# Kernel optimization log

Hardware: AMD Instinct MI355X
Metric: run time of the kernel (lower is better)

Reference implementation:

```python
import jax, jax.numpy as jnp
import numpy as np

N_CLASSES = 80
SEG_LEN = 512          # boxes per class (uniform segments)
H = 128                # hidden_size
DH = 2 * H             # decoder hidden (= concat of bidirectional encoder final hiddens)
EMB = 32               # decoder_input_dim
SOS, EOS = 2, 3


def _gru_cell(x, h, Wih, Whh, bih, bhh):
    # PyTorch GRU cell math. x:(in,), h:(hid,), Wih:(3*hid,in), Whh:(3*hid,hid)
    gi = Wih @ x + bih
    gh = Whh @ h + bhh
    i_r, i_z, i_n = jnp.split(gi, 3)
    h_r, h_z, h_n = jnp.split(gh, 3)
    r = jax.nn.sigmoid(i_r + h_r)
    z = jax.nn.sigmoid(i_z + h_z)
    n = jnp.tanh(i_n + r * h_n)
    return (1.0 - z) * n + z * h


def _gru_seq(xs, h0, Wih, Whh, bih, bhh):
    # xs: (T, in); returns final hidden (hid,) and all hiddens (T, hid)
    def step(h, x):
        h2 = _gru_cell(x, h, Wih, Whh, bih, bhh)
        return h2, h2
    hT, hs = jax.lax.scan(step, h0, xs)
    return hT, hs

# vmap over the 80 classes (per-class weights)
_run_gru = jax.vmap(_gru_seq, in_axes=(0, 0, 0, 0, 0, 0))


def setup_inputs() -> dict:
    key = jax.random.key(0)
    ks = jax.random.split(key, 32)
    N = N_CLASSES * SEG_LEN
    s = 0.05
    inp = {
        "feat": jax.random.normal(ks[0], (N, 1024), jnp.float32),
        "score": jax.random.uniform(ks[1], (N, 1), jnp.float32),
        "box": jax.random.uniform(ks[2], (N, 4), jnp.float32),
        "origin_score": jax.random.uniform(ks[3], (N, 91), jnp.float32),
        "labels": jax.random.randint(ks[4], (N,), 0, 2, jnp.int64),
        "weights": jax.random.uniform(ks[5], (N,), jnp.float32),
        "unique_class": jnp.ones((N_CLASSES,), jnp.int64),
        "unique_class_len": jnp.arange(N_CLASSES + 1, dtype=jnp.int64) * SEG_LEN,
        # shared linears
        "appear_W": jax.random.normal(ks[6], (H, 1024), jnp.float32) * s,
        "appear_b": jnp.zeros((H,), jnp.float32),
        "featlin_W": jax.random.normal(ks[7], (H, H + 96), jnp.float32) * s,
        "featlin_b": jnp.zeros((H,), jnp.float32),
        # per-class bidirectional encoder GRUs
        "enc_Wih_f": jax.random.normal(ks[8], (N_CLASSES, 3 * H, H), jnp.float32) * s,
        "enc_Whh_f": jax.random.normal(ks[9], (N_CLASSES, 3 * H, H), jnp.float32) * s,
        "enc_bih_f": jnp.zeros((N_CLASSES, 3 * H), jnp.float32),
        "enc_bhh_f": jnp.zeros((N_CLASSES, 3 * H), jnp.float32),
        "enc_Wih_b": jax.random.normal(ks[10], (N_CLASSES, 3 * H, H), jnp.float32) * s,
        "enc_Whh_b": jax.random.normal(ks[11], (N_CLASSES, 3 * H, H), jnp.float32) * s,
        "enc_bih_b": jnp.zeros((N_CLASSES, 3 * H), jnp.float32),
        "enc_bhh_b": jnp.zeros((N_CLASSES, 3 * H), jnp.float32),
        # decoder
        "dec_emb": jax.random.normal(ks[12], (4, EMB), jnp.float32) * s,
        "dec_Wih": jax.random.normal(ks[13], (N_CLASSES, 3 * DH, EMB), jnp.float32) * s,
        "dec_Whh": jax.random.normal(ks[14], (N_CLASSES, 3 * DH, DH), jnp.float32) * s,
        "dec_bih": jnp.zeros((N_CLASSES, 3 * DH), jnp.float32),
        "dec_bhh": jnp.zeros((N_CLASSES, 3 * DH), jnp.float32),
        "out_W": jax.random.normal(ks[15], (4, DH), jnp.float32) * s,
        "out_b": jnp.zeros((4,), jnp.float32),
    }
    return inp


def reference(feat, score, box, origin_score, labels, weights, unique_class,
              unique_class_len, appear_W, appear_b, featlin_W, featlin_b,
              enc_Wih_f, enc_Whh_f, enc_bih_f, enc_bhh_f,
              enc_Wih_b, enc_Whh_b, enc_bih_b, enc_bhh_b,
              dec_emb, dec_Wih, dec_Whh, dec_bih, dec_bhh, out_W, out_b):
    # --- shared feature encoding ---
    x = jax.nn.relu(feat @ appear_W.T + appear_b)                    # (N, H)
    allf = jnp.concatenate([x, score, box, origin_score], axis=1)    # (N, H+96)
    enc_feat = jax.nn.relu(allf @ featlin_W.T + featlin_b)           # (N, H)

    # --- per-class bidirectional encoder (uniform segments) ---
    seg = enc_feat.reshape(N_CLASSES, SEG_LEN, H)
    eos = jnp.ones((N_CLASSES, 1, H), enc_feat.dtype)                # encoder_EOS = ones
    enc_in = jnp.concatenate([seg, eos], axis=1)                     # (80, L+1, H)
    h0 = jnp.zeros((N_CLASSES, H), enc_feat.dtype)
    h_f, _ = _run_gru(enc_in, h0, enc_Wih_f, enc_Whh_f, enc_bih_f, enc_bhh_f)
    h_b, _ = _run_gru(enc_in[:, ::-1], h0, enc_Wih_b, enc_Whh_b, enc_bih_b, enc_bhh_b)
    dec_h0 = jnp.concatenate([h_f, h_b], axis=-1)                    # (80, 2H)

    # --- per-class decoder with teacher forcing (SOS then gold labels) ---
    emb = dec_emb[labels].reshape(N_CLASSES, SEG_LEN, EMB)
    sos = jnp.broadcast_to(dec_emb[SOS], (N_CLASSES, 1, EMB))
    dec_in = jnp.concatenate([sos, emb], axis=1)                     # (80, L+1, EMB)
    _, dec_hs = _run_gru(dec_in, dec_h0, dec_Wih, dec_Whh, dec_bih, dec_bhh)

    logits = dec_hs.reshape(-1, DH) @ out_W.T + out_b                # (80*(L+1), 4)
    output = jax.nn.log_softmax(logits, axis=-1)
    return output, labels, weights
```

## Files before the change

### kernel.cpp

```cpp
#include <hip/hip_runtime.h>


typedef __fp16 h2v __attribute__((ext_vector_type(2)));

#define HAVE_FDOT2 1

__device__ __forceinline__ h2v pk2(float a, float b) {
  return __builtin_amdgcn_cvt_pkrtz(a, b);
}
__device__ __forceinline__ unsigned h2u(h2v h) { return __builtin_bit_cast(unsigned, h); }
__device__ __forceinline__ h2v u2h(unsigned u) { return __builtin_bit_cast(h2v, u); }
__device__ __forceinline__ float fdot2f(h2v a, h2v b, float c) {
#if HAVE_FDOT2 && __has_builtin(__builtin_amdgcn_fdot2)
  return __builtin_amdgcn_fdot2(a, b, c, false);
#else
  return c + (float)a.x * (float)b.x + (float)a.y * (float)b.y;
#endif
}
__device__ __forceinline__ float sigf(float x) { return 1.f / (1.f + __expf(-x)); }
__device__ __forceinline__ float tanhfast(float x) { return 2.f / (1.f + __expf(-2.f * x)) - 1.f; }

__global__ void k_fill_misc(const float* __restrict__ score, const float* __restrict__ box,
                            const float* __restrict__ orig, float* __restrict__ allf) {
  int i = blockIdx.x * blockDim.x + threadIdx.x;
  if (i >= 40960 * 96) return;
  int row = i / 96, k = i - row * 96;
  float v;
  if (k == 0) v = score[row];
  else if (k < 5) v = box[row * 4 + (k - 1)];
  else v = orig[(size_t)row * 91 + (k - 5)];
  allf[(size_t)row * 224 + 128 + k] = v;
}

__global__ __launch_bounds__(256) void k_gemm_appear(
    const float* __restrict__ A, const float* __restrict__ W,
    const float* __restrict__ bias, float* __restrict__ allf) {
  __shared__ float As[32][68];
  __shared__ float Ws[32][132];
  const int tid = threadIdx.x;
  const int tx = tid & 15, ty = tid >> 4;
  const int r0 = blockIdx.x * 64;
  const int lr = tid >> 3;
  const int lk = (tid & 7) * 4;
  float acc[4][8];
#pragma unroll
  for (int i = 0; i < 4; ++i)
#pragma unroll
    for (int j = 0; j < 8; ++j) acc[i][j] = 0.f;

  for (int k0 = 0; k0 < 1024; k0 += 32) {
#pragma unroll
    for (int i = 0; i < 2; ++i) {
      int rr = lr + i * 32;
      float4 v = *(const float4*)(A + (size_t)(r0 + rr) * 1024 + k0 + lk);
      As[lk + 0][rr] = v.x; As[lk + 1][rr] = v.y; As[lk + 2][rr] = v.z; As[lk + 3][rr] = v.w;
    }
#pragma unroll
    for (int i = 0; i < 4; ++i) {
      int wr = lr + i * 32;
      float4 v = *(const float4*)(W + (size_t)wr * 1024 + k0 + lk);
      Ws[lk + 0][wr] = v.x; Ws[lk + 1][wr] = v.y; Ws[lk + 2][wr] = v.z; Ws[lk + 3][wr] = v.w;
    }
    __syncthreads();
#pragma unroll
    for (int kk = 0; kk < 32; ++kk) {
      float4 a = *(const float4*)&As[kk][ty * 4];
      float4 w0 = *(const float4*)&Ws[kk][tx * 8];
      float4 w1 = *(const float4*)&Ws[kk][tx * 8 + 4];
      float av[4] = {a.x, a.y, a.z, a.w};
      float wv[8] = {w0.x, w0.y, w0.z, w0.w, w1.x, w1.y, w1.z, w1.w};
#pragma unroll
      for (int i = 0; i < 4; ++i)
#pragma unroll
        for (int j = 0; j < 8; ++j) acc[i][j] = fmaf(av[i], wv[j], acc[i][j]);
    }
    __syncthreads();
  }
#pragma unroll
  for (int i = 0; i < 4; ++i) {
    int row = r0 + ty * 4 + i;
#pragma unroll
    for (int j = 0; j < 8; ++j) {
      int col = tx * 8 + j;
      float v = acc[i][j] + bias[col];
      allf[(size_t)row * 224 + col] = fmaxf(v, 0.f);
    }
  }
}

__global__ __launch_bounds__(256) void k_gemm_featlin(
    const float* __restrict__ A, const float* __restrict__ W,
    const float* __restrict__ bias, unsigned* __restrict__ encf2) {
  __shared__ float As[32][68];
  __shared__ float Ws[32][132];
  const int tid = threadIdx.x;
  const int tx = tid & 15, ty = tid >> 4;
  const int r0 = blockIdx.x * 64;
  const int lr = tid >> 3;
  const int lk = (tid & 7) * 4;
  float acc[4][8];
#pragma unroll
  for (int i = 0; i < 4; ++i)
#pragma unroll
    for (int j = 0; j < 8; ++j) acc[i][j] = 0.f;

  for (int k0 = 0; k0 < 224; k0 += 32) {
#pragma unroll
    for (int i = 0; i < 2; ++i) {
      int rr = lr + i * 32;
      float4 v = *(const float4*)(A + (size_t)(r0 + rr) * 224 + k0 + lk);
      As[lk + 0][rr] = v.x; As[lk + 1][rr] = v.y; As[lk + 2][rr] = v.z; As[lk + 3][rr] = v.w;
    }
#pragma unroll
    for (int i = 0; i < 4; ++i) {
      int wr = lr + i * 32;
      float4 v = *(const float4*)(W + (size_t)wr * 224 + k0 + lk);
      Ws[lk + 0][wr] = v.x; Ws[lk + 1][wr] = v.y; Ws[lk + 2][wr] = v.z; Ws[lk + 3][wr] = v.w;
    }
    __syncthreads();
#pragma unroll
    for (int kk = 0; kk < 32; ++kk) {
      float4 a = *(const float4*)&As[kk][ty * 4];
      float4 w0 = *(const float4*)&Ws[kk][tx * 8];
      float4 w1 = *(const float4*)&Ws[kk][tx * 8 + 4];
      float av[4] = {a.x, a.y, a.z, a.w};
      float wv[8] = {w0.x, w0.y, w0.z, w0.w, w1.x, w1.y, w1.z, w1.w};
#pragma unroll
      for (int i = 0; i < 4; ++i)
#pragma unroll
        for (int j = 0; j < 8; ++j) acc[i][j] = fmaf(av[i], wv[j], acc[i][j]);
    }
    __syncthreads();
  }
#pragma unroll
  for (int i = 0; i < 4; ++i) {
    int row = r0 + ty * 4 + i;
    unsigned* orow = encf2 + (size_t)row * 64;
#pragma unroll
    for (int p = 0; p < 4; ++p) {
      int col = tx * 8 + 2 * p;
      float a = fmaxf(acc[i][2 * p] + bias[col], 0.f);
      float b = fmaxf(acc[i][2 * p + 1] + bias[col + 1], 0.f);
      orow[tx * 4 + p] = h2u(pk2(a, b));
    }
  }
}

__global__ __launch_bounds__(256) void k_dec_gi(
    const float* __restrict__ Wih, const float* __restrict__ bih,
    const float* __restrict__ emb, float* __restrict__ gi) {
  __shared__ float e[4][32];
  const int c = blockIdx.x, tid = threadIdx.x;
  if (tid < 128) e[tid >> 5][tid & 31] = emb[tid];
  __syncthreads();
#pragma unroll
  for (int i = 0; i < 3; ++i) {
    int r = tid + i * 256;
    const float* w = Wih + ((size_t)c * 768 + r) * 32;
    float b = bih[(size_t)c * 768 + r];
    float a0 = b, a1 = b, a2 = b, a3 = b;
#pragma unroll
    for (int k = 0; k < 32; ++k) {
      float wv = w[k];
      a0 = fmaf(wv, e[0][k], a0);
      a1 = fmaf(wv, e[1][k], a1);
      a2 = fmaf(wv, e[2][k], a2);
      a3 = fmaf(wv, e[3][k], a3);
    }
    gi[((size_t)c * 4 + 0) * 768 + r] = a0;
    gi[((size_t)c * 4 + 1) * 768 + r] = a1;
    gi[((size_t)c * 4 + 2) * 768 + r] = a2;
    gi[((size_t)c * 4 + 3) * 768 + r] = a3;
  }
}

__global__ __launch_bounds__(512) void k_enc_gru(
    const unsigned* __restrict__ encf2,
    const float* __restrict__ WihF, const float* __restrict__ WhhF,
    const float* __restrict__ bihF, const float* __restrict__ bhhF,
    const float* __restrict__ WihB, const float* __restrict__ WhhB,
    const float* __restrict__ bihB, const float* __restrict__ bhhB,
    float* __restrict__ dec_h0) {
  const int blk = blockIdx.x;
  const int c = blk >> 1, dir = blk & 1;
  const int tid = threadIdx.x;

  const float* Wih = (dir ? WihB : WihF) + (size_t)c * 384 * 128;
  const float* Whh = (dir ? WhhB : WhhF) + (size_t)c * 384 * 128;
  const float* bih = (dir ? bihB : bihF) + (size_t)c * 384;
  const float* bhh = (dir ? bhhB : bhhF) + (size_t)c * 384;

  __shared__ __align__(16) unsigned x2s[2][64];
  __shared__ __align__(16) unsigned h2s[64];
  __shared__ float iis[384];
  __shared__ float hhs[384];

  h2v wih[64], whh[64];
  float bi = 0.f, bh = 0.f;
  if (tid < 384) {
    const float4* w4 = (const float4*)(Wih + (size_t)tid * 128);
#pragma unroll
    for (int k = 0; k < 32; ++k) {
      float4 v = w4[k];
      wih[2 * k] = pk2(v.x, v.y);
      wih[2 * k + 1] = pk2(v.z, v.w);
    }
    const float4* u4 = (const float4*)(Whh + (size_t)tid * 128);
#pragma unroll
    for (int k = 0; k < 32; ++k) {
      float4 v = u4[k];
      whh[2 * k] = pk2(v.x, v.y);
      whh[2 * k + 1] = pk2(v.z, v.w);
    }
    bi = bih[tid];
    bh = bhh[tid];
  }
  if (tid < 64) h2s[tid] = 0u;
  if (tid >= 448) {
    int lane = tid - 448;
    x2s[0][lane] = (dir == 0) ? encf2[((size_t)c * 512 + 0) * 64 + lane] : 0x3C003C00u;
  }
  float hreg = 0.f;
  __syncthreads();

  for (int t = 0; t <= 512; ++t) {
    if (tid < 384) {
      float aI = bi, aH = bh;
      const uint4* xp = (const uint4*)(&x2s[t & 1][0]);
      const uint4* hp = (const uint4*)(&h2s[0]);
#pragma unroll
      for (int k = 0; k < 16; ++k) {
        uint4 x = xp[k];
        aI = fdot2f(wih[4 * k + 0], u2h(x.x), aI);
        aI = fdot2f(wih[4 * k + 1], u2h(x.y), aI);
        aI = fdot2f(wih[4 * k + 2], u2h(x.z), aI);
        aI = fdot2f(wih[4 * k + 3], u2h(x.w), aI);
      }
#pragma unroll
      for (int k = 0; k < 16; ++k) {
        uint4 h = hp[k];
        aH = fdot2f(whh[4 * k + 0], u2h(h.x), aH);
        aH = fdot2f(whh[4 * k + 1], u2h(h.y), aH);
        aH = fdot2f(whh[4 * k + 2], u2h(h.z), aH);
        aH = fdot2f(whh[4 * k + 3], u2h(h.w), aH);
      }
      iis[tid] = aI;
      hhs[tid] = aH;
    } else if (tid >= 448) {
      if (t < 512) {
        int tn = t + 1, lane = tid - 448;
        int row;
        if (dir == 0) row = (tn < 512) ? tn : -1;
        else row = 512 - tn;
        x2s[tn & 1][lane] = (row < 0) ? 0x3C003C00u
                                      : encf2[((size_t)c * 512 + row) * 64 + lane];
      }
    }
    __syncthreads();
    if (tid < 128) {
      float rg = sigf(iis[tid] + hhs[tid]);
      float z = sigf(iis[128 + tid] + hhs[128 + tid]);
      float nn = tanhfast(iis[256 + tid] + rg * hhs[256 + tid]);
      float hn = (1.f - z) * nn + z * hreg;
      hreg = hn;
      float other = __shfl_xor(hn, 1, 64);
      if ((tid & 1) == 0) h2s[tid >> 1] = h2u(pk2(hn, other));
    }
    __syncthreads();
  }
  if (tid < 128) dec_h0[(size_t)c * 256 + dir * 128 + tid] = hreg;
}

__global__ __launch_bounds__(768) void k_dec_gru(
    const float* __restrict__ Whh, const float* __restrict__ bhh,
    const float* __restrict__ gi, const float* __restrict__ h0,
    const int* __restrict__ labels,
    const float* __restrict__ outW, const float* __restrict__ outB,
    float* __restrict__ out) {
  const int c = blockIdx.x, tid = threadIdx.x;
  __shared__ __align__(16) unsigned h2s[128];
  __shared__ float gsum[512];
  __shared__ float gni[256], gnh[256];
  __shared__ int labs[512];
  __shared__ float red[4][4];

  h2v whh[128];
  {
    const float4* w4 = (const float4*)(Whh + ((size_t)c * 768 + tid) * 256);
#pragma unroll
    for (int k = 0; k < 64; ++k) {
      float4 v = w4[k];
      whh[2 * k] = pk2(v.x, v.y);
      whh[2 * k + 1] = pk2(v.z, v.w);
    }
  }
  float bh = bhh[(size_t)c * 768 + tid];
  float g0 = gi[((size_t)c * 4 + 0) * 768 + tid];
  float g1 = gi[((size_t)c * 4 + 1) * 768 + tid];
  float g2 = gi[((size_t)c * 4 + 2) * 768 + tid];
  if (tid < 512) labs[tid] = labels[(size_t)c * 512 + tid];
  float b0 = outB[0], b1 = outB[1], b2 = outB[2], b3 = outB[3];
  float hreg = 0.f, ow0 = 0.f, ow1 = 0.f, ow2 = 0.f, ow3 = 0.f;
  if (tid < 256) {
    hreg = h0[(size_t)c * 256 + tid];
    ow0 = outW[tid];
    ow1 = outW[256 + tid];
    ow2 = outW[512 + tid];
    ow3 = outW[768 + tid];
    float other = __shfl_xor(hreg, 1, 64);
    if ((tid & 1) == 0) h2s[tid >> 1] = h2u(pk2(hreg, other));
  }
  __syncthreads();

  for (int t = 0; t <= 512; ++t) {
    {
      float aH = bh;
      const uint4* hp = (const uint4*)(&h2s[0]);
#pragma unroll
      for (int k = 0; k < 32; ++k) {
        uint4 h = hp[k];
        aH = fdot2f(whh[4 * k + 0], u2h(h.x), aH);
        aH = fdot2f(whh[4 * k + 1], u2h(h.y), aH);
        aH = fdot2f(whh[4 * k + 2], u2h(h.z), aH);
        aH = fdot2f(whh[4 * k + 3], u2h(h.w), aH);
      }
      float ii = (t == 0) ? g2 : (labs[t - 1] ? g1 : g0);
      if (tid < 512) gsum[tid] = ii + aH;
      else {
        gni[tid - 512] = ii;
        gnh[tid - 512] = aH;
      }
    }
    __syncthreads();
    if (tid < 256) {
      float rg = sigf(gsum[tid]);
      float z = sigf(gsum[256 + tid]);
      float nn = tanhfast(gni[tid] + rg * gnh[tid]);
      float hn = (1.f - z) * nn + z * hreg;
      hreg = hn;
      float other = __shfl_xor(hn, 1, 64);
      if ((tid & 1) == 0) h2s[tid >> 1] = h2u(pk2(hn, other));
      float p0 = ow0 * hn, p1 = ow1 * hn, p2 = ow2 * hn, p3 = ow3 * hn;
#pragma unroll
      for (int off = 32; off > 0; off >>= 1) {
        p0 += __shfl_xor(p0, off, 64);
        p1 += __shfl_xor(p1, off, 64);
        p2 += __shfl_xor(p2, off, 64);
        p3 += __shfl_xor(p3, off, 64);
      }
      if ((tid & 63) == 0) {
        int w = tid >> 6;
        red[w][0] = p0; red[w][1] = p1; red[w][2] = p2; red[w][3] = p3;
      }
    }
    __syncthreads();
    if (tid == 0) {
      float l0 = red[0][0] + red[1][0] + red[2][0] + red[3][0] + b0;
      float l1 = red[0][1] + red[1][1] + red[2][1] + red[3][1] + b1;
      float l2 = red[0][2] + red[1][2] + red[2][2] + red[3][2] + b2;
      float l3 = red[0][3] + red[1][3] + red[2][3] + red[3][3] + b3;
      float m = fmaxf(fmaxf(l0, l1), fmaxf(l2, l3));
      float s = __expf(l0 - m) + __expf(l1 - m) + __expf(l2 - m) + __expf(l3 - m);
      float lse = m + __logf(s);
      float* o = out + ((size_t)c * 513 + t) * 4;
      o[0] = l0 - lse; o[1] = l1 - lse; o[2] = l2 - lse; o[3] = l3 - lse;
    }
  }
}

__global__ void k_passthrough(const int* __restrict__ labels,
                              const float* __restrict__ weights,
                              float* __restrict__ out) {
  int i = blockIdx.x * blockDim.x + threadIdx.x;
  if (i < 40960) {
    out[164160 + i] = (float)labels[i];
    out[164160 + 40960 + i] = weights[i];
  }
}

extern "C" void kernel_launch(void* const* d_in, const int* in_sizes, int n_in,
                              void* d_out, int out_size, void* d_ws, size_t ws_size,
                              hipStream_t stream) {
  (void)in_sizes; (void)n_in; (void)out_size; (void)ws_size;
  const float* feat = (const float*)d_in[0];
  const float* score = (const float*)d_in[1];
  const float* box = (const float*)d_in[2];
  const float* orig = (const float*)d_in[3];
  const int* labels = (const int*)d_in[4];
  const float* weights = (const float*)d_in[5];
  const float* appear_W = (const float*)d_in[8];
  const float* appear_b = (const float*)d_in[9];
  const float* featlin_W = (const float*)d_in[10];
  const float* featlin_b = (const float*)d_in[11];
  const float* eWihF = (const float*)d_in[12];
  const float* eWhhF = (const float*)d_in[13];
  const float* ebihF = (const float*)d_in[14];
  const float* ebhhF = (const float*)d_in[15];
  const float* eWihB = (const float*)d_in[16];
  const float* eWhhB = (const float*)d_in[17];
  const float* ebihB = (const float*)d_in[18];
  const float* ebhhB = (const float*)d_in[19];
  const float* dec_emb = (const float*)d_in[20];
  const float* dWih = (const float*)d_in[21];
  const float* dWhh = (const float*)d_in[22];
  const float* dbih = (const float*)d_in[23];
  const float* dbhh = (const float*)d_in[24];
  const float* outW = (const float*)d_in[25];
  const float* outB = (const float*)d_in[26];
  float* out = (float*)d_out;

  char* ws = (char*)d_ws;
  float* allf = (float*)ws;
  unsigned* encf2 = (unsigned*)(ws + (size_t)40960 * 224 * 4);
  float* dec_h0 = (float*)(ws + (size_t)40960 * 224 * 4 + (size_t)40960 * 64 * 4);
  float* dec_gi = dec_h0 + 80 * 256;

  k_fill_misc<<<15360, 256, 0, stream>>>(score, box, orig, allf);
  k_gemm_appear<<<640, 256, 0, stream>>>(feat, appear_W, appear_b, allf);
  k_gemm_featlin<<<640, 256, 0, stream>>>(allf, featlin_W, featlin_b, encf2);
  k_dec_gi<<<80, 256, 0, stream>>>(dWih, dbih, dec_emb, dec_gi);
  k_enc_gru<<<160, 512, 0, stream>>>(encf2, eWihF, eWhhF, ebihF, ebhhF,
                                     eWihB, eWhhB, ebihB, ebhhB, dec_h0);
  k_dec_gru<<<80, 768, 0, stream>>>(dWhh, dbhh, dec_gi, dec_h0, labels, outW, outB, out);
  k_passthrough<<<160, 256, 0, stream>>>(labels, weights, out);
}
```

Before: 1.666 ms.

## Split GRU matvecs across lanes with DPP reductions in encoder and decoder

Reworks the per-step matrix-vector products in both the encoder and decoder GRU kernels. Instead of one thread computing a full dot product over the hidden vector, each group of 16 lanes splits the K dimension and combines partial sums with DPP and swizzle cross-lane reductions. This shortens the serial dependency chain per timestep and uses all 512 encoder threads for compute. The encoder also fuses the r/z input and hidden sums and moves the x prefetch store after the barrier. The decoder stages the gate inputs and output weights in shared memory and adds occupancy hints to the launch bounds, at the cost of more cross-lane shuffle work and register pressure.

```diff
diff --git a/kernel.cpp b/kernel.cpp
--- a/kernel.cpp
+++ b/kernel.cpp
@@ -2,8 +2,6 @@
 
 
 typedef __fp16 h2v __attribute__((ext_vector_type(2)));
-
-#define HAVE_FDOT2 1
 
 __device__ __forceinline__ h2v pk2(float a, float b) {
   return __builtin_amdgcn_cvt_pkrtz(a, b);
@@ -11,14 +9,31 @@
 __device__ __forceinline__ unsigned h2u(h2v h) { return __builtin_bit_cast(unsigned, h); }
 __device__ __forceinline__ h2v u2h(unsigned u) { return __builtin_bit_cast(h2v, u); }
 __device__ __forceinline__ float fdot2f(h2v a, h2v b, float c) {
-#if HAVE_FDOT2 && __has_builtin(__builtin_amdgcn_fdot2)
   return __builtin_amdgcn_fdot2(a, b, c, false);
-#else
-  return c + (float)a.x * (float)b.x + (float)a.y * (float)b.y;
-#endif
 }
 __device__ __forceinline__ float sigf(float x) { return 1.f / (1.f + __expf(-x)); }
 __device__ __forceinline__ float tanhfast(float x) { return 2.f / (1.f + __expf(-2.f * x)) - 1.f; }
+
+template <int CTRL>
+__device__ __forceinline__ float dppadd(float acc, float v) {
+  int r = __builtin_amdgcn_update_dpp(0, __float_as_int(v), CTRL, 0xF, 0xF, true);
+  return acc + __int_as_float(r);
+}
+__device__ __forceinline__ float swz4add(float acc, float v) {
+  return acc + __int_as_float(__builtin_amdgcn_ds_swizzle(__float_as_int(v), 0x101F));
+}
+
+__device__ __forceinline__ float reduce8(float p[8]) {
+  p[0] = dppadd<0xB1>(p[0], p[1]);
+  p[2] = dppadd<0xB1>(p[2], p[3]);
+  p[4] = dppadd<0xB1>(p[4], p[5]);
+  p[6] = dppadd<0xB1>(p[6], p[7]);
+  p[0] = dppadd<0x4E>(p[0], p[2]);
+  p[4] = dppadd<0x4E>(p[4], p[6]);
+  p[0] = swz4add(p[0], p[4]);
+  p[0] = dppadd<0x128>(p[0], p[0]);
+  return p[0];
+}
 
 __global__ void k_fill_misc(const float* __restrict__ score, const float* __restrict__ box,
                             const float* __restrict__ orig, float* __restrict__ allf) {
@@ -174,7 +189,7 @@
   }
 }
 
-__global__ __launch_bounds__(512) void k_enc_gru(
+__global__ __launch_bounds__(512, 2) void k_enc_gru(
     const unsigned* __restrict__ encf2,
     const float* __restrict__ WihF, const float* __restrict__ WhhF,
     const float* __restrict__ bihF, const float* __restrict__ bhhF,
@@ -184,6 +199,7 @@
   const int blk = blockIdx.x;
   const int c = blk >> 1, dir = blk & 1;
   const int tid = threadIdx.x;
+  const int w = tid >> 6, l = tid & 63, q = l >> 4, m = l & 15, mw = m & 7;
 
   const float* Wih = (dir ? WihB : WihF) + (size_t)c * 384 * 128;
   const float* Whh = (dir ? WhhB : WhhF) + (size_t)c * 384 * 128;
@@ -192,29 +208,39 @@
 
   __shared__ __align__(16) unsigned x2s[2][64];
   __shared__ __align__(16) unsigned h2s[64];
-  __shared__ float iis[384];
-  __shared__ float hhs[384];
-
-  h2v wih[64], whh[64];
-  float bi = 0.f, bh = 0.f;
-  if (tid < 384) {
-    const float4* w4 = (const float4*)(Wih + (size_t)tid * 128);
-#pragma unroll
-    for (int k = 0; k < 32; ++k) {
-      float4 v = w4[k];
-      wih[2 * k] = pk2(v.x, v.y);
-      wih[2 * k + 1] = pk2(v.z, v.w);
-    }
-    const float4* u4 = (const float4*)(Whh + (size_t)tid * 128);
-#pragma unroll
-    for (int k = 0; k < 32; ++k) {
-      float4 v = u4[k];
-      whh[2 * k] = pk2(v.x, v.y);
-      whh[2 * k + 1] = pk2(v.z, v.w);
-    }
-    bi = bih[tid];
-    bh = bhh[tid];
-  }
+  __shared__ float aBuf[512];
+
+  h2v wci[8][4], wch[8][4], wsg[8][4];
+#pragma unroll
+  for (int k = 0; k < 8; ++k) {
+    int vc = 32 * w + 8 * q + (k ^ mw);
+    const float4* pi = (const float4*)(Wih + (size_t)vc * 128 + 8 * m);
+    float4 a = pi[0], b = pi[1];
+    wci[k][0] = pk2(a.x, a.y); wci[k][1] = pk2(a.z, a.w);
+    wci[k][2] = pk2(b.x, b.y); wci[k][3] = pk2(b.z, b.w);
+    const float4* ph = (const float4*)(Whh + (size_t)vc * 128 + 8 * m);
+    float4 e = ph[0], f = ph[1];
+    wch[k][0] = pk2(e.x, e.y); wch[k][1] = pk2(e.z, e.w);
+    wch[k][2] = pk2(f.x, f.y); wch[k][3] = pk2(f.z, f.w);
+    int s = (w < 4) ? (32 * w + 8 * q + (k ^ mw)) : (32 * (w - 4) + 8 * q + (k ^ mw));
+    const float* sb = (w < 4) ? (Wih + (size_t)(256 + s) * 128) : (Whh + (size_t)(256 + s) * 128);
+    const float4* ps = (const float4*)(sb + 8 * m);
+    float4 g = ps[0], hh = ps[1];
+    wsg[k][0] = pk2(g.x, g.y); wsg[k][1] = pk2(g.z, g.w);
+    wsg[k][2] = pk2(hh.x, hh.y); wsg[k][3] = pk2(hh.z, hh.w);
+  }
+  float bown;
+  int ownIdx;
+  if (m < 8) {
+    int vo = 32 * w + 8 * q + m;
+    bown = bih[vo] + bhh[vo];
+    ownIdx = vo;
+  } else {
+    int so = (w < 4) ? (32 * w + 8 * q + mw) : (32 * (w - 4) + 8 * q + mw);
+    bown = (w < 4) ? bih[256 + so] : bhh[256 + so];
+    ownIdx = (w < 4) ? (256 + so) : (384 + so);
+  }
+
   if (tid < 64) h2s[tid] = 0u;
   if (tid >= 448) {
     int lane = tid - 448;
@@ -224,123 +250,151 @@
   __syncthreads();
 
   for (int t = 0; t <= 512; ++t) {
-    if (tid < 384) {
-      float aI = bi, aH = bh;
-      const uint4* xp = (const uint4*)(&x2s[t & 1][0]);
-      const uint4* hp = (const uint4*)(&h2s[0]);
-#pragma unroll
-      for (int k = 0; k < 16; ++k) {
-        uint4 x = xp[k];
-        aI = fdot2f(wih[4 * k + 0], u2h(x.x), aI);
-        aI = fdot2f(wih[4 * k + 1], u2h(x.y), aI);
-        aI = fdot2f(wih[4 * k + 2], u2h(x.z), aI);
-        aI = fdot2f(wih[4 * k + 3], u2h(x.w), aI);
-      }
-#pragma unroll
-      for (int k = 0; k < 16; ++k) {
-        uint4 h = hp[k];
-        aH = fdot2f(whh[4 * k + 0], u2h(h.x), aH);
-        aH = fdot2f(whh[4 * k + 1], u2h(h.y), aH);
-        aH = fdot2f(whh[4 * k + 2], u2h(h.z), aH);
-        aH = fdot2f(whh[4 * k + 3], u2h(h.w), aH);
-      }
-      iis[tid] = aI;
-      hhs[tid] = aH;
-    } else if (tid >= 448) {
-      if (t < 512) {
-        int tn = t + 1, lane = tid - 448;
-        int row;
-        if (dir == 0) row = (tn < 512) ? tn : -1;
-        else row = 512 - tn;
-        x2s[tn & 1][lane] = (row < 0) ? 0x3C003C00u
-                                      : encf2[((size_t)c * 512 + row) * 64 + lane];
-      }
-    }
+    unsigned xpre = 0;
+    if (tid >= 448 && t < 512) {
+      int tn = t + 1, lane = tid - 448;
+      int row = (dir == 0) ? ((tn < 512) ? tn : -1) : (512 - tn);
+      xpre = (row < 0) ? 0x3C003C00u : encf2[((size_t)c * 512 + row) * 64 + lane];
+    }
+    uint4 xv = ((const uint4*)&x2s[t & 1][0])[m];
+    uint4 hv = ((const uint4*)&h2s[0])[m];
+    h2v x0 = u2h(xv.x), x1 = u2h(xv.y), x2 = u2h(xv.z), x3 = u2h(xv.w);
+    h2v g0 = u2h(hv.x), g1 = u2h(hv.y), g2 = u2h(hv.z), g3 = u2h(hv.w);
+    float pA, pB;
+    {
+      float p[8];
+#pragma unroll
+      for (int k = 0; k < 8; ++k) {
+        float a = 0.f;
+        a = fdot2f(wci[k][0], x0, a); a = fdot2f(wci[k][1], x1, a);
+        a = fdot2f(wci[k][2], x2, a); a = fdot2f(wci[k][3], x3, a);
+        a = fdot2f(wch[k][0], g0, a); a = fdot2f(wch[k][1], g1, a);
+        a = fdot2f(wch[k][2], g2, a); a = fdot2f(wch[k][3], g3, a);
+        p[k] = a;
+      }
+      pA = reduce8(p);
+    }
+    {
+      h2v s0 = (w < 4) ? x0 : g0, s1 = (w < 4) ? x1 : g1;
+      h2v s2 = (w < 4) ? x2 : g2, s3 = (w < 4) ? x3 : g3;
+      float p[8];
+#pragma unroll
+      for (int k = 0; k < 8; ++k) {
+        float a = 0.f;
+        a = fdot2f(wsg[k][0], s0, a); a = fdot2f(wsg[k][1], s1, a);
+        a = fdot2f(wsg[k][2], s2, a); a = fdot2f(wsg[k][3], s3, a);
+        p[k] = a;
+      }
+      pB = reduce8(p);
+    }
+    aBuf[ownIdx] = ((m < 8) ? pA : pB) + bown;
     __syncthreads();
     if (tid < 128) {
-      float rg = sigf(iis[tid] + hhs[tid]);
-      float z = sigf(iis[128 + tid] + hhs[128 + tid]);
-      float nn = tanhfast(iis[256 + tid] + rg * hhs[256 + tid]);
+      float r = sigf(aBuf[tid]);
+      float z = sigf(aBuf[128 + tid]);
+      float nn = tanhfast(aBuf[256 + tid] + r * aBuf[384 + tid]);
       float hn = (1.f - z) * nn + z * hreg;
       hreg = hn;
       float other = __shfl_xor(hn, 1, 64);
       if ((tid & 1) == 0) h2s[tid >> 1] = h2u(pk2(hn, other));
+    } else if (tid >= 448 && t < 512) {
+      x2s[(t + 1) & 1][tid - 448] = xpre;
     }
     __syncthreads();
   }
   if (tid < 128) dec_h0[(size_t)c * 256 + dir * 128 + tid] = hreg;
 }
 
-__global__ __launch_bounds__(768) void k_dec_gru(
+__global__ __launch_bounds__(768, 3) void k_dec_gru(
     const float* __restrict__ Whh, const float* __restrict__ bhh,
     const float* __restrict__ gi, const float* __restrict__ h0,
     const int* __restrict__ labels,
     const float* __restrict__ outW, const float* __restrict__ outB,
     float* __restrict__ out) {
   const int c = blockIdx.x, tid = threadIdx.x;
+  const int w = tid >> 6, l = tid & 63, q = l >> 4, m = l & 15, mw = m & 7;
+
   __shared__ __align__(16) unsigned h2s[128];
-  __shared__ float gsum[512];
-  __shared__ float gni[256], gnh[256];
-  __shared__ int labs[512];
+  __shared__ float aBuf[768];
+  __shared__ float gisf[2304];
+  __shared__ float owsh[1024];
+  __shared__ int labs[513];
   __shared__ float red[4][4];
 
-  h2v whh[128];
-  {
-    const float4* w4 = (const float4*)(Whh + ((size_t)c * 768 + tid) * 256);
-#pragma unroll
-    for (int k = 0; k < 64; ++k) {
-      float4 v = w4[k];
-      whh[2 * k] = pk2(v.x, v.y);
-      whh[2 * k + 1] = pk2(v.z, v.w);
-    }
-  }
-  float bh = bhh[(size_t)c * 768 + tid];
-  float g0 = gi[((size_t)c * 4 + 0) * 768 + tid];
-  float g1 = gi[((size_t)c * 4 + 1) * 768 + tid];
-  float g2 = gi[((size_t)c * 4 + 2) * 768 + tid];
-  if (tid < 512) labs[tid] = labels[(size_t)c * 512 + tid];
+  h2v wpk[2][8][8];
+#pragma unroll
+  for (int kc = 0; kc < 2; ++kc)
+#pragma unroll
+    for (int k = 0; k < 8; ++k) {
+      int row = 64 * w + 16 * q + 8 * kc + (k ^ mw);
+      const float4* src = (const float4*)(Whh + ((size_t)c * 768 + row) * 256 + 16 * m);
+      float4 v0 = src[0], v1 = src[1], v2 = src[2], v3 = src[3];
+      wpk[kc][k][0] = pk2(v0.x, v0.y); wpk[kc][k][1] = pk2(v0.z, v0.w);
+      wpk[kc][k][2] = pk2(v1.x, v1.y); wpk[kc][k][3] = pk2(v1.z, v1.w);
+      wpk[kc][k][4] = pk2(v2.x, v2.y); wpk[kc][k][5] = pk2(v2.z, v2.w);
+      wpk[kc][k][6] = pk2(v3.x, v3.y); wpk[kc][k][7] = pk2(v3.z, v3.w);
+    }
+  float bown = bhh[(size_t)c * 768 + 64 * w + l];
+
+  for (int i = tid; i < 2304; i += 768) gisf[i] = gi[(size_t)c * 4 * 768 + i];
+  for (int i = tid; i < 1024; i += 768) owsh[i] = outW[i];
+  if (tid < 512) labs[tid + 1] = labels[(size_t)c * 512 + tid];
+  if (tid == 512) labs[0] = 2;
   float b0 = outB[0], b1 = outB[1], b2 = outB[2], b3 = outB[3];
-  float hreg = 0.f, ow0 = 0.f, ow1 = 0.f, ow2 = 0.f, ow3 = 0.f;
+  float hreg = 0.f;
   if (tid < 256) {
     hreg = h0[(size_t)c * 256 + tid];
-    ow0 = outW[tid];
-    ow1 = outW[256 + tid];
-    ow2 = outW[512 + tid];
-    ow3 = outW[768 + tid];
     float other = __shfl_xor(hreg, 1, 64);
     if ((tid & 1) == 0) h2s[tid >> 1] = h2u(pk2(hreg, other));
   }
   __syncthreads();
 
   for (int t = 0; t <= 512; ++t) {
+    const uint4* hp = (const uint4*)(&h2s[0]);
+    uint4 ha = hp[2 * m], hb = hp[2 * m + 1];
+    h2v g0 = u2h(ha.x), g1 = u2h(ha.y), g2 = u2h(ha.z), g3 = u2h(ha.w);
+    h2v g4 = u2h(hb.x), g5 = u2h(hb.y), g6 = u2h(hb.z), g7 = u2h(hb.w);
+    float pc0, pc1;
     {
-      float aH = bh;
-      const uint4* hp = (const uint4*)(&h2s[0]);
-#pragma unroll
-      for (int k = 0; k < 32; ++k) {
-        uint4 h = hp[k];
-        aH = fdot2f(whh[4 * k + 0], u2h(h.x), aH);
-        aH = fdot2f(whh[4 * k + 1], u2h(h.y), aH);
-        aH = fdot2f(whh[4 * k + 2], u2h(h.z), aH);
-        aH = fdot2f(whh[4 * k + 3], u2h(h.w), aH);
-      }
-      float ii = (t == 0) ? g2 : (labs[t - 1] ? g1 : g0);
-      if (tid < 512) gsum[tid] = ii + aH;
-      else {
-        gni[tid - 512] = ii;
-        gnh[tid - 512] = aH;
-      }
-    }
+      float p[8];
+#pragma unroll
+      for (int k = 0; k < 8; ++k) {
+        float a = 0.f;
+        a = fdot2f(wpk[0][k][0], g0, a); a = fdot2f(wpk[0][k][1], g1, a);
+        a = fdot2f(wpk[0][k][2], g2, a); a = fdot2f(wpk[0][k][3], g3, a);
+        a = fdot2f(wpk[0][k][4], g4, a); a = fdot2f(wpk[0][k][5], g5, a);
+        a = fdot2f(wpk[0][k][6], g6, a); a = fdot2f(wpk[0][k][7], g7, a);
+        p[k] = a;
+      }
+      pc0 = reduce8(p);
+    }
+    {
+      float p[8];
+#pragma unroll
+      for (int k = 0; k < 8; ++k) {
+        float a = 0.f;
+        a = fdot2f(wpk[1][k][0], g0, a); a = fdot2f(wpk[1][k][1], g1, a);
+        a = fdot2f(wpk[1][k][2], g2, a); a = fdot2f(wpk[1][k][3], g3, a);
+        a = fdot2f(wpk[1][k][4], g4, a); a = fdot2f(wpk[1][k][5], g5, a);
+        a = fdot2f(wpk[1][k][6], g6, a); a = fdot2f(wpk[1][k][7], g7, a);
+        p[k] = a;
+      }
+      pc1 = reduce8(p);
+    }
+    aBuf[64 * w + l] = ((m < 8) ? pc0 : pc1) + bown;
     __syncthreads();
     if (tid < 256) {
-      float rg = sigf(gsum[tid]);
-      float z = sigf(gsum[256 + tid]);
-      float nn = tanhfast(gni[tid] + rg * gnh[tid]);
+      int sel = labs[t];
+      const float* gsel = &gisf[sel * 768];
+      float r = sigf(gsel[tid] + aBuf[tid]);
+      float z = sigf(gsel[256 + tid] + aBuf[256 + tid]);
+      float nn = tanhfast(gsel[512 + tid] + r * aBuf[512 + tid]);
       float hn = (1.f - z) * nn + z * hreg;
       hreg = hn;
       float other = __shfl_xor(hn, 1, 64);
       if ((tid & 1) == 0) h2s[tid >> 1] = h2u(pk2(hn, other));
-      float p0 = ow0 * hn, p1 = ow1 * hn, p2 = ow2 * hn, p3 = ow3 * hn;
+      float p0 = owsh[tid] * hn, p1 = owsh[256 + tid] * hn;
+      float p2 = owsh[512 + tid] * hn, p3 = owsh[768 + tid] * hn;
 #pragma unroll
       for (int off = 32; off > 0; off >>= 1) {
         p0 += __shfl_xor(p0, off, 64);
@@ -349,8 +403,8 @@
         p3 += __shfl_xor(p3, off, 64);
       }
       if ((tid & 63) == 0) {
-        int w = tid >> 6;
-        red[w][0] = p0; red[w][1] = p1; red[w][2] = p2; red[w][3] = p3;
+        int ww = tid >> 6;
+        red[ww][0] = p0; red[ww][1] = p1; red[ww][2] = p2; red[ww][3] = p3;
       }
     }
     __syncthreads();
@@ -359,9 +413,9 @@
       float l1 = red[0][1] + red[1][1] + red[2][1] + red[3][1] + b1;
       float l2 = red[0][2] + red[1][2] + red[2][2] + red[3][2] + b2;
       float l3 = red[0][3] + red[1][3] + red[2][3] + red[3][3] + b3;
-      float m = fmaxf(fmaxf(l0, l1), fmaxf(l2, l3));
-      float s = __expf(l0 - m) + __expf(l1 - m) + __expf(l2 - m) + __expf(l3 - m);
-      float lse = m + __logf(s);
+      float mm = fmaxf(fmaxf(l0, l1), fmaxf(l2, l3));
+      float s = __expf(l0 - mm) + __expf(l1 - mm) + __expf(l2 - mm) + __expf(l3 - mm);
+      float lse = mm + __logf(s);
       float* o = out + ((size_t)c * 513 + t) * 4;
       o[0] = l0 - lse; o[1] = l1 - lse; o[2] = l2 - lse; o[3] = l3 - lse;
     }
```

Result: no change. 1.652 ms (-0.8%).
